# Kernel optimization log

Hardware: AMD Instinct MI355X
Metric: run time of the kernel (lower is better)

The kernel has to match this reference:

```python
import jax, jax.numpy as jnp
import numpy as np

N_BLOCKS = 4
DIN = 4000      # features per input block
DE = 128        # embed dims per block
DLAT = 512      # latent dim per block
ALPHA = 0.3     # Keras LeakyReLU default negative slope


def setup_inputs() -> dict:
    key = jax.random.key(0)
    ks = jax.random.split(key, 7)
    N = 4096
    x = jax.random.normal(ks[0], (N, N_BLOCKS * DIN), dtype=jnp.float32)
    mask = jax.random.bernoulli(ks[1], 0.5, (N, N_BLOCKS * DIN))
    embed = jax.random.normal(ks[2], (N, N_BLOCKS * DE), dtype=jnp.float32)
    batches = jax.random.normal(ks[3], (N, 8), dtype=jnp.float32)
    mean_vals = jax.random.normal(ks[4], (N_BLOCKS * DIN,), dtype=jnp.float32)
    fan_in = DIN + DE + 8
    W = jax.random.normal(ks[5], (N_BLOCKS, fan_in, DLAT), dtype=jnp.float32) / np.sqrt(fan_in)
    b = jnp.zeros((N_BLOCKS, DLAT), dtype=jnp.float32)
    return {"x": x, "mask": mask, "embed": embed, "batches": batches,
            "mean_vals": mean_vals, "W": W, "b": b}


def reference(x, mask, embed, batches, mean_vals, W, b):
    N = x.shape[0]
    db = batches.shape[1]
    # masked mean-centering: x = where(mask, x - mean, 0)
    xm = jnp.where(mask, x - mean_vals[None, :], jnp.zeros((), x.dtype))
    # equal-sized splits == reshape into [N, B, din] / [N, B, de]
    xb = xm.reshape(N, N_BLOCKS, DIN)
    eb = embed.reshape(N, N_BLOCKS, DE)
    bb = jnp.broadcast_to(batches[:, None, :], (N, N_BLOCKS, db))
    inp = jnp.concatenate([xb, eb, bb], axis=-1)  # [N, B, DIN+DE+db]
    h = jnp.einsum('nbi,bio->nbo', inp, W) + b[None, :, :]  # grouped GEMM
    h = jnp.where(h >= 0, h, ALPHA * h)  # LeakyReLU(alpha=0.3)
    return h.reshape(N, N_BLOCKS * DLAT)  # concat of per-block outputs
```

## Files before the change

### kernel.cpp

```cpp
#include <hip/hip_runtime.h>

#define NROWS 4096
#define NBLK 4
#define DIN 4000
#define DE 128
#define DB 8
#define DLAT 512
#define FANIN 4136
#define KPAD 4224
#define NKT 66
#define XC 16000
#define OUTC 2048
#define TC 192

#define PW_GRID 2112

typedef __attribute__((ext_vector_type(8))) short short8;
typedef __attribute__((ext_vector_type(4))) float floatx4;
typedef float __attribute__((ext_vector_type(4))) f32x4;
typedef int   __attribute__((ext_vector_type(4))) i32x4;

__device__ __forceinline__ unsigned short f2bf(float f) {
    unsigned int u = __builtin_bit_cast(unsigned int, f);
    u = (u + 0x7FFFu + ((u >> 16) & 1u)) >> 16;
    return (unsigned short)u;
}

__device__ __forceinline__ void async16(const void* g, void* l) {
    __builtin_amdgcn_global_load_lds(
        (const __attribute__((address_space(1))) void*)g,
        (__attribute__((address_space(3))) void*)l, 16, 0, 0);
}

__global__ void prep_w(const float* __restrict__ W, unsigned short* __restrict__ Wp) {
    __shared__ unsigned short tile[64 * 68];
    int bid = blockIdx.x;
    int nt = bid & 7;
    int t2 = bid >> 3;
    int kt = t2 % 66;
    int b  = t2 / 66;
    int tid = threadIdx.x;
    int n0 = nt * 64;
    int k0 = kt * 64;
#pragma unroll
    for (int i = 0; i < 4; ++i) {
        int c = i * 256 + tid;
        int r = c >> 4;
        int q = (c & 15) * 4;
        int pk = k0 + r;
        int wr = (pk < DIN) ? pk : ((pk >= 4032 && pk < 4168) ? pk - 32 : -1);
        float4 v = make_float4(0.f, 0.f, 0.f, 0.f);
        if (wr >= 0)
            v = *reinterpret_cast<const float4*>(W + ((size_t)b * FANIN + wr) * DLAT + n0 + q);
        ushort4 u4 = make_ushort4(f2bf(v.x), f2bf(v.y), f2bf(v.z), f2bf(v.w));
        *reinterpret_cast<ushort4*>(&tile[r * 68 + q]) = u4;
    }
    __syncthreads();
#pragma unroll
    for (int i = 0; i < 2; ++i) {
        int c = i * 256 + tid;
        int nl = c >> 3;
        int kc = c & 7;
        unsigned short o[8];
#pragma unroll
        for (int j = 0; j < 8; ++j) o[j] = tile[(kc * 8 + j) * 68 + nl];
        *reinterpret_cast<short8*>(Wp + ((size_t)(b * DLAT + n0 + nl)) * KPAD + k0 + kc * 8) =
            *reinterpret_cast<const short8*>(o);
    }
}

__global__ __launch_bounds__(512, 2) void gemm_f(
    const float* __restrict__ x, const int* __restrict__ mask,
    const float* __restrict__ mean, const float* __restrict__ embed,
    const float* __restrict__ batches, const float* __restrict__ bias,
    const unsigned short* __restrict__ Wp, float* __restrict__ out) {
    __shared__ unsigned short A0[64 * 64];
    __shared__ unsigned short A1[64 * 64];
    __shared__ unsigned short B0[512 * 64];
    __shared__ unsigned short B1[512 * 64];

    int bid = blockIdx.x;
    int b   = bid & 3;
    int mt  = bid >> 2;
    int row0 = mt * 64;
    int tid  = threadIdx.x;
    int lane = tid & 63;
    int w    = tid >> 6;
    int quad = lane >> 4;
    int l16  = lane & 15;
    int r    = tid >> 3;
    int cgl  = tid & 7;

    const unsigned short* Bbase = Wp + (size_t)b * DLAT * KPAD;

    floatx4 acc[4][4];
#pragma unroll
    for (int m = 0; m < 4; ++m)
#pragma unroll
        for (int n = 0; n < 4; ++n) acc[m][n] = (floatx4){0.f, 0.f, 0.f, 0.f};

    f32x4 xa, xb, ea, eb;
    i32x4 mka, mkb;
    int amode;

#define STAGE_B(BN, KT) do {                                                   \
    int k0_ = (KT) * 64;                                                       \
    _Pragma("unroll")                                                          \
    for (int i_ = 0; i_ < 8; ++i_) {                                           \
        int c_  = i_ * 512 + tid;                                              \
        int nl_ = c_ >> 3;                                                     \
        int cg_ = (c_ & 7) ^ (nl_ & 7);                                        \
        async16(Bbase + (size_t)nl_ * KPAD + k0_ + cg_ * 8, &BN[c_ * 8]);      \
    }                                                                          \
} while (0)

#define LOAD_A(KT) do {                                                        \
    int col_ = (KT) * 64 + cgl * 8;                                            \
    amode = 3;                                                                 \
    if (col_ < DIN) {                                                          \
        amode = 0;                                                             \
        size_t gi_ = (size_t)(row0 + r) * XC + (size_t)b * DIN + col_;         \
        const f32x4* xp_ = reinterpret_cast<const f32x4*>(x + gi_);            \
        const i32x4* mp_ = reinterpret_cast<const i32x4*>(mask + gi_);         \
        xa  = __builtin_nontemporal_load(xp_);                                 \
        xb  = __builtin_nontemporal_load(xp_ + 1);                             \
        mka = __builtin_nontemporal_load(mp_);                                 \
        mkb = __builtin_nontemporal_load(mp_ + 1);                             \
        const f32x4* ep_ = reinterpret_cast<const f32x4*>(mean + b * DIN + col_); \
        ea = ep_[0]; eb = ep_[1];                                              \
    } else if (col_ >= 4032 && col_ < 4160) {                                  \
        amode = 1;                                                             \
        const f32x4* ep_ = reinterpret_cast<const f32x4*>(                     \
            embed + (size_t)(row0 + r) * (NBLK * DE) + b * DE + (col_ - 4032)); \
        ea = ep_[0]; eb = ep_[1];                                              \
    } else if (col_ == 4160) {                                                 \
        amode = 1;                                                             \
        const f32x4* bp_ = reinterpret_cast<const f32x4*>(                     \
            batches + (size_t)(row0 + r) * DB);                                \
        ea = bp_[0]; eb = bp_[1];                                              \
    }                                                                          \
} while (0)

#define WRITE_A(AN) do {                                                       \
    short8 v8_ = (short8){0, 0, 0, 0, 0, 0, 0, 0};                             \
    if (amode == 0) {                                                          \
        float f0_ = mka.x ? xa.x - ea.x : 0.f;                                 \
        float f1_ = mka.y ? xa.y - ea.y : 0.f;                                 \
        float f2_ = mka.z ? xa.z - ea.z : 0.f;                                 \
        float f3_ = mka.w ? xa.w - ea.w : 0.f;                                 \
        float f4_ = mkb.x ? xb.x - eb.x : 0.f;                                 \
        float f5_ = mkb.y ? xb.y - eb.y : 0.f;                                 \
        float f6_ = mkb.z ? xb.z - eb.z : 0.f;                                 \
        float f7_ = mkb.w ? xb.w - eb.w : 0.f;                                 \
        v8_ = (short8){(short)f2bf(f0_), (short)f2bf(f1_), (short)f2bf(f2_),   \
                       (short)f2bf(f3_), (short)f2bf(f4_), (short)f2bf(f5_),   \
                       (short)f2bf(f6_), (short)f2bf(f7_)};                    \
    } else if (amode == 1) {                                                   \
        v8_ = (short8){(short)f2bf(ea.x), (short)f2bf(ea.y), (short)f2bf(ea.z),\
                       (short)f2bf(ea.w), (short)f2bf(eb.x), (short)f2bf(eb.y),\
                       (short)f2bf(eb.z), (short)f2bf(eb.w)};                  \
    }                                                                          \
    *reinterpret_cast<short8*>(&AN[r * 64 + ((cgl ^ (r & 7)) * 8)]) = v8_;     \
} while (0)

#define COMPUTE(AN, BN) do {                                                   \
    _Pragma("unroll")                                                          \
    for (int s_ = 0; s_ < 2; ++s_) {                                           \
        short8 af_[4], bf_[4];                                                 \
        _Pragma("unroll")                                                      \
        for (int m_ = 0; m_ < 4; ++m_) {                                       \
            int ar_ = m_ * 16 + l16;                                           \
            af_[m_] = *reinterpret_cast<const short8*>(                        \
                &AN[ar_ * 64 + (((s_ * 4 + quad) ^ (ar_ & 7)) * 8)]);          \
        }                                                                      \
        _Pragma("unroll")                                                      \
        for (int n_ = 0; n_ < 4; ++n_) {                                       \
            int br_ = w * 64 + n_ * 16 + l16;                                  \
            bf_[n_] = *reinterpret_cast<const short8*>(                        \
                &BN[br_ * 64 + (((s_ * 4 + quad) ^ (br_ & 7)) * 8)]);          \
        }                                                                      \
        _Pragma("unroll")                                                      \
        for (int m_ = 0; m_ < 4; ++m_)                                         \
            _Pragma("unroll")                                                  \
            for (int n_ = 0; n_ < 4; ++n_)                                     \
                acc[m_][n_] = __builtin_amdgcn_mfma_f32_16x16x32_bf16(         \
                    af_[m_], bf_[n_], acc[m_][n_], 0, 0, 0);                   \
    }                                                                          \
} while (0)

    LOAD_A(0);
    STAGE_B(B0, 0);
    WRITE_A(A0);
    __syncthreads();

    for (int kt = 0; kt < NKT; kt += 2) {
        LOAD_A(kt + 1);
        STAGE_B(B1, kt + 1);
        COMPUTE(A0, B0);
        WRITE_A(A1);
        __syncthreads();
        if (kt + 2 < NKT) {
            LOAD_A(kt + 2);
            STAGE_B(B0, kt + 2);
        }
        COMPUTE(A1, B1);
        if (kt + 2 < NKT) WRITE_A(A0);
        __syncthreads();
    }

#pragma unroll
    for (int m = 0; m < 4; ++m) {
#pragma unroll
        for (int n = 0; n < 4; ++n) {
            int col_l = w * 64 + n * 16 + l16;
            float bv = bias[b * DLAT + col_l];
#pragma unroll
            for (int rr = 0; rr < 4; ++rr) {
                int row_l = m * 16 + quad * 4 + rr;
                float v = acc[m][n][rr] + bv;
                v = v >= 0.f ? v : 0.3f * v;
                out[(size_t)(row0 + row_l) * OUTC + b * DLAT + col_l] = v;
            }
        }
    }
#undef STAGE_B
#undef LOAD_A
#undef WRITE_A
#undef COMPUTE
}

__global__ void prep_t(const float* __restrict__ embed, const float* __restrict__ batches,
                       unsigned short* __restrict__ T) {
    int i  = blockIdx.x * 256 + threadIdx.x;
    int t  = i % TC;
    int nb = i / TC;
    int b  = nb & 3;
    int n  = nb >> 2;
    float v = 0.f;
    if (t < DE)            v = embed[(size_t)n * (NBLK * DE) + b * DE + t];
    else if (t < DE + DB)  v = batches[(size_t)n * DB + (t - DE)];
    T[i] = f2bf(v);
}

__global__ __launch_bounds__(256, 3) void gemm_k(
    const float* __restrict__ x, const int* __restrict__ mask,
    const float* __restrict__ mean, const float* __restrict__ bias,
    const unsigned short* __restrict__ Wp, const unsigned short* __restrict__ T,
    float* __restrict__ out) {
    __shared__ unsigned short Asm_[128 * 64];
    __shared__ unsigned short Bsm_[128 * 64];

    int bid = blockIdx.x;
    int nt  = bid & 3;
    int b   = (bid >> 2) & 3;
    int mt  = bid >> 4;
    int tid  = threadIdx.x;
    int lane = tid & 63;
    int w    = tid >> 6;
    int wm   = w >> 1;
    int wn   = w & 1;
    int quad = lane >> 4;
    int l16  = lane & 15;
    int row0 = mt * 128;
    int n0   = nt * 128;

    floatx4 acc[4][4];
#pragma unroll
    for (int m = 0; m < 4; ++m)
#pragma unroll
        for (int n = 0; n < 4; ++n) acc[m][n] = (floatx4){0.f, 0.f, 0.f, 0.f};

    for (int kt = 0; kt < NKT; ++kt) {
        if (kt < 63) {
#pragma unroll
            for (int i = 0; i < 4; ++i) {
                int c  = i * 256 + tid;
                int r  = c >> 3;
                int cg = c & 7;
                int col = kt * 64 + cg * 8;
                short8 v8 = (short8){0, 0, 0, 0, 0, 0, 0, 0};
                if (col < DIN) {
                    size_t gi = (size_t)(row0 + r) * XC + (size_t)b * DIN + col;
                    const float4* xp = reinterpret_cast<const float4*>(x + gi);
                    const int4*   mp = reinterpret_cast<const int4*>(mask + gi);
                    const float4* ep = reinterpret_cast<const float4*>(mean + b * DIN + col);
                    float4 x0 = xp[0], x1 = xp[1];
                    int4   m0 = mp[0], m1 = mp[1];
                    float4 e0 = ep[0], e1 = ep[1];
                    float f0 = m0.x ? x0.x - e0.x : 0.f;
                    float f1 = m0.y ? x0.y - e0.y : 0.f;
                    float f2 = m0.z ? x0.z - e0.z : 0.f;
                    float f3 = m0.w ? x0.w - e0.w : 0.f;
                    float f4 = m1.x ? x1.x - e1.x : 0.f;
                    float f5 = m1.y ? x1.y - e1.y : 0.f;
                    float f6 = m1.z ? x1.z - e1.z : 0.f;
                    float f7 = m1.w ? x1.w - e1.w : 0.f;
                    v8 = (short8){(short)f2bf(f0), (short)f2bf(f1), (short)f2bf(f2),
                                  (short)f2bf(f3), (short)f2bf(f4), (short)f2bf(f5),
                                  (short)f2bf(f6), (short)f2bf(f7)};
                }
                *reinterpret_cast<short8*>(&Asm_[r * 64 + ((cg ^ (r & 7)) * 8)]) = v8;
            }
        } else {
#pragma unroll
            for (int i = 0; i < 4; ++i) {
                int c  = i * 256 + tid;
                int r  = c >> 3;
                int cg = (c & 7) ^ (r & 7);
                async16(T + ((size_t)(row0 + r) * NBLK + b) * TC + (kt - 63) * 64 + cg * 8,
                        &Asm_[c * 8]);
            }
        }
#pragma unroll
        for (int i = 0; i < 4; ++i) {
            int c  = i * 256 + tid;
            int nl = c >> 3;
            int cg = (c & 7) ^ (nl & 7);
            async16(Wp + ((size_t)(b * DLAT + n0 + nl)) * KPAD + kt * 64 + cg * 8,
                    &Bsm_[c * 8]);
        }
        __syncthreads();
#pragma unroll
        for (int s = 0; s < 2; ++s) {
            short8 af[4], bfr[4];
#pragma unroll
            for (int m = 0; m < 4; ++m) {
                int ar = wm * 64 + m * 16 + l16;
                af[m] = *reinterpret_cast<const short8*>(
                    &Asm_[ar * 64 + (((s * 4 + quad) ^ (ar & 7)) * 8)]);
            }
#pragma unroll
            for (int n = 0; n < 4; ++n) {
                int br = wn * 64 + n * 16 + l16;
                bfr[n] = *reinterpret_cast<const short8*>(
                    &Bsm_[br * 64 + (((s * 4 + quad) ^ (br & 7)) * 8)]);
            }
#pragma unroll
            for (int m = 0; m < 4; ++m)
#pragma unroll
                for (int n = 0; n < 4; ++n)
                    acc[m][n] = __builtin_amdgcn_mfma_f32_16x16x32_bf16(
                        af[m], bfr[n], acc[m][n], 0, 0, 0);
        }
        __syncthreads();
    }

#pragma unroll
    for (int m = 0; m < 4; ++m) {
#pragma unroll
        for (int n = 0; n < 4; ++n) {
            int col_l = wn * 64 + n * 16 + l16;
            float bv = bias[b * DLAT + n0 + col_l];
#pragma unroll
            for (int r = 0; r < 4; ++r) {
                int row_l = wm * 64 + m * 16 + quad * 4 + r;
                float v = acc[m][n][r] + bv;
                v = v >= 0.f ? v : 0.3f * v;
                out[(size_t)(row0 + row_l) * OUTC + b * DLAT + n0 + col_l] = v;
            }
        }
    }
}

extern "C" void kernel_launch(void* const* d_in, const int* in_sizes, int n_in,
                              void* d_out, int out_size, void* d_ws, size_t ws_size,
                              hipStream_t stream) {
    const float* x       = (const float*)d_in[0];
    const int*   mask    = (const int*)d_in[1];
    const float* embed   = (const float*)d_in[2];
    const float* batches = (const float*)d_in[3];
    const float* mean    = (const float*)d_in[4];
    const float* W       = (const float*)d_in[5];
    const float* bias    = (const float*)d_in[6];
    float* out = (float*)d_out;

    unsigned short* Wp = (unsigned short*)d_ws;
    size_t wp_elems = (size_t)NBLK * DLAT * KPAD;
    size_t wp_bytes = wp_elems * 2;

    prep_w<<<dim3(PW_GRID), dim3(256), 0, stream>>>(W, Wp);

    if (ws_size >= wp_bytes + (size_t)(NROWS * NBLK * TC) * 2) {
        gemm_f<<<dim3(256), dim3(512), 0, stream>>>(
            x, mask, mean, embed, batches, bias, Wp, out);
    } else {
        unsigned short* T = Wp + wp_elems;
        prep_t<<<dim3(12288), dim3(256), 0, stream>>>(embed, batches, T);
        gemm_k<<<dim3(512), dim3(256), 0, stream>>>(x, mask, mean, bias, Wp, T, out);
    }
}
```

Measured before the change: 601.3 us.

## Precompute tail A tiles in prep kernel and hand-schedule GEMM pipeline waits

The weight-prep kernel now also writes a bf16 tensor holding the last four K-tiles of A: the final masked-x columns, embed and batches. The GEMM reads those tiles with async LDS loads, so its main loop no longer carries the branchy amode logic. The main loop is restructured to issue the next A global load before the barrier. It replaces __syncthreads with explicit vmcnt/lgkmcnt waits and sched_barriers, which lets loads stay in flight across the MFMA phase. This adds some extra workspace traffic, and the manual waitcnt counts have to match the exact number of outstanding loads.

Result: faster. 584.7 us (-2.8%).

```diff
diff --git a/kernel.cpp b/kernel.cpp
--- a/kernel.cpp
+++ b/kernel.cpp
@@ -12,8 +12,10 @@
 #define XC 16000
 #define OUTC 2048
 #define TC 192
+#define T2C 256
 
 #define PW_GRID 2112
+#define PT2_GRID 2048
 
 typedef __attribute__((ext_vector_type(8))) short short8;
 typedef __attribute__((ext_vector_type(4))) float floatx4;
@@ -32,48 +34,101 @@
         (__attribute__((address_space(3))) void*)l, 16, 0, 0);
 }
 
-__global__ void prep_w(const float* __restrict__ W, unsigned short* __restrict__ Wp) {
+#define SCHED0 __builtin_amdgcn_sched_barrier(0)
+#define BAR    __builtin_amdgcn_s_barrier()
+#define WAITVM6 asm volatile("s_waitcnt vmcnt(6)" ::: "memory")
+#define WAITVM0 asm volatile("s_waitcnt vmcnt(0)" ::: "memory")
+#define WAITLG  asm volatile("s_waitcnt lgkmcnt(0)" ::: "memory")
+
+__global__ void prep_wt(const float* __restrict__ W, unsigned short* __restrict__ Wp,
+                        const float* __restrict__ x, const int* __restrict__ mask,
+                        const float* __restrict__ mean, const float* __restrict__ embed,
+                        const float* __restrict__ batches, unsigned short* __restrict__ T2) {
     __shared__ unsigned short tile[64 * 68];
     int bid = blockIdx.x;
-    int nt = bid & 7;
-    int t2 = bid >> 3;
-    int kt = t2 % 66;
-    int b  = t2 / 66;
     int tid = threadIdx.x;
-    int n0 = nt * 64;
-    int k0 = kt * 64;
-#pragma unroll
-    for (int i = 0; i < 4; ++i) {
-        int c = i * 256 + tid;
-        int r = c >> 4;
-        int q = (c & 15) * 4;
-        int pk = k0 + r;
-        int wr = (pk < DIN) ? pk : ((pk >= 4032 && pk < 4168) ? pk - 32 : -1);
-        float4 v = make_float4(0.f, 0.f, 0.f, 0.f);
-        if (wr >= 0)
-            v = *reinterpret_cast<const float4*>(W + ((size_t)b * FANIN + wr) * DLAT + n0 + q);
-        ushort4 u4 = make_ushort4(f2bf(v.x), f2bf(v.y), f2bf(v.z), f2bf(v.w));
-        *reinterpret_cast<ushort4*>(&tile[r * 68 + q]) = u4;
-    }
-    __syncthreads();
-#pragma unroll
-    for (int i = 0; i < 2; ++i) {
-        int c = i * 256 + tid;
-        int nl = c >> 3;
-        int kc = c & 7;
-        unsigned short o[8];
-#pragma unroll
-        for (int j = 0; j < 8; ++j) o[j] = tile[(kc * 8 + j) * 68 + nl];
-        *reinterpret_cast<short8*>(Wp + ((size_t)(b * DLAT + n0 + nl)) * KPAD + k0 + kc * 8) =
-            *reinterpret_cast<const short8*>(o);
-    }
+
+    if (bid < PW_GRID) {
+        int nt = bid & 7;
+        int t2 = bid >> 3;
+        int kt = t2 % 66;
+        int b  = t2 / 66;
+        int n0 = nt * 64;
+        int k0 = kt * 64;
+#pragma unroll
+        for (int i = 0; i < 4; ++i) {
+            int c = i * 256 + tid;
+            int r = c >> 4;
+            int q = (c & 15) * 4;
+            int pk = k0 + r;
+            int wr = (pk < DIN) ? pk : ((pk >= 4032 && pk < 4168) ? pk - 32 : -1);
+            float4 v = make_float4(0.f, 0.f, 0.f, 0.f);
+            if (wr >= 0)
+                v = *reinterpret_cast<const float4*>(W + ((size_t)b * FANIN + wr) * DLAT + n0 + q);
+            ushort4 u4 = make_ushort4(f2bf(v.x), f2bf(v.y), f2bf(v.z), f2bf(v.w));
+            *reinterpret_cast<ushort4*>(&tile[r * 68 + q]) = u4;
+        }
+        __syncthreads();
+#pragma unroll
+        for (int i = 0; i < 2; ++i) {
+            int c = i * 256 + tid;
+            int nl = c >> 3;
+            int kc = c & 7;
+            unsigned short o[8];
+#pragma unroll
+            for (int j = 0; j < 8; ++j) o[j] = tile[(kc * 8 + j) * 68 + nl];
+            *reinterpret_cast<short8*>(Wp + ((size_t)(b * DLAT + n0 + nl)) * KPAD + k0 + kc * 8) =
+                *reinterpret_cast<const short8*>(o);
+        }
+        return;
+    }
+
+    int i  = (bid - PW_GRID) * 256 + tid;
+    int tc = i & 31;
+    int rb = i >> 5;
+    int b  = rb & 3;
+    int row = rb >> 2;
+    int k  = tc * 8;
+    short8 v8 = (short8){0, 0, 0, 0, 0, 0, 0, 0};
+    if (k < 32) {
+        int col = 3968 + k;
+        size_t gi = (size_t)row * XC + (size_t)b * DIN + col;
+        const f32x4* xp = reinterpret_cast<const f32x4*>(x + gi);
+        const i32x4* mp = reinterpret_cast<const i32x4*>(mask + gi);
+        const f32x4* ep = reinterpret_cast<const f32x4*>(mean + b * DIN + col);
+        f32x4 x0 = xp[0], x1 = xp[1];
+        i32x4 m0 = mp[0], m1 = mp[1];
+        f32x4 e0 = ep[0], e1 = ep[1];
+        float f0 = m0.x ? x0.x - e0.x : 0.f;
+        float f1 = m0.y ? x0.y - e0.y : 0.f;
+        float f2 = m0.z ? x0.z - e0.z : 0.f;
+        float f3 = m0.w ? x0.w - e0.w : 0.f;
+        float f4 = m1.x ? x1.x - e1.x : 0.f;
+        float f5 = m1.y ? x1.y - e1.y : 0.f;
+        float f6 = m1.z ? x1.z - e1.z : 0.f;
+        float f7 = m1.w ? x1.w - e1.w : 0.f;
+        v8 = (short8){(short)f2bf(f0), (short)f2bf(f1), (short)f2bf(f2), (short)f2bf(f3),
+                      (short)f2bf(f4), (short)f2bf(f5), (short)f2bf(f6), (short)f2bf(f7)};
+    } else if (k >= 64 && k < 192) {
+        const f32x4* ep = reinterpret_cast<const f32x4*>(
+            embed + (size_t)row * (NBLK * DE) + b * DE + (k - 64));
+        f32x4 a = ep[0], bb = ep[1];
+        v8 = (short8){(short)f2bf(a.x), (short)f2bf(a.y), (short)f2bf(a.z), (short)f2bf(a.w),
+                      (short)f2bf(bb.x), (short)f2bf(bb.y), (short)f2bf(bb.z), (short)f2bf(bb.w)};
+    } else if (k == 192) {
+        const f32x4* bp = reinterpret_cast<const f32x4*>(batches + (size_t)row * DB);
+        f32x4 a = bp[0], bb = bp[1];
+        v8 = (short8){(short)f2bf(a.x), (short)f2bf(a.y), (short)f2bf(a.z), (short)f2bf(a.w),
+                      (short)f2bf(bb.x), (short)f2bf(bb.y), (short)f2bf(bb.z), (short)f2bf(bb.w)};
+    }
+    *reinterpret_cast<short8*>(T2 + (size_t)rb * T2C + k) = v8;
 }
 
 __global__ __launch_bounds__(512, 2) void gemm_f(
     const float* __restrict__ x, const int* __restrict__ mask,
-    const float* __restrict__ mean, const float* __restrict__ embed,
-    const float* __restrict__ batches, const float* __restrict__ bias,
-    const unsigned short* __restrict__ Wp, float* __restrict__ out) {
+    const float* __restrict__ mean, const float* __restrict__ bias,
+    const unsigned short* __restrict__ Wp, const unsigned short* __restrict__ T2,
+    float* __restrict__ out) {
     __shared__ unsigned short A0[64 * 64];
     __shared__ unsigned short A1[64 * 64];
     __shared__ unsigned short B0[512 * 64];
@@ -101,7 +156,6 @@
 
     f32x4 xa, xb, ea, eb;
     i32x4 mka, mkb;
-    int amode;
 
 #define STAGE_B(BN, KT) do {                                                   \
     int k0_ = (KT) * 64;                                                       \
@@ -114,52 +168,37 @@
     }                                                                          \
 } while (0)
 
+#define STAGE_T(AN, KT) do {                                                   \
+    async16(T2 + ((size_t)(row0 + r) * NBLK + b) * T2C + ((KT) - 62) * 64 +    \
+                ((cgl ^ (r & 7)) * 8),                                         \
+            &AN[tid * 8]);                                                     \
+} while (0)
+
 #define LOAD_A(KT) do {                                                        \
     int col_ = (KT) * 64 + cgl * 8;                                            \
-    amode = 3;                                                                 \
-    if (col_ < DIN) {                                                          \
-        amode = 0;                                                             \
-        size_t gi_ = (size_t)(row0 + r) * XC + (size_t)b * DIN + col_;         \
-        const f32x4* xp_ = reinterpret_cast<const f32x4*>(x + gi_);            \
-        const i32x4* mp_ = reinterpret_cast<const i32x4*>(mask + gi_);         \
-        xa  = __builtin_nontemporal_load(xp_);                                 \
-        xb  = __builtin_nontemporal_load(xp_ + 1);                             \
-        mka = __builtin_nontemporal_load(mp_);                                 \
-        mkb = __builtin_nontemporal_load(mp_ + 1);                             \
-        const f32x4* ep_ = reinterpret_cast<const f32x4*>(mean + b * DIN + col_); \
-        ea = ep_[0]; eb = ep_[1];                                              \
-    } else if (col_ >= 4032 && col_ < 4160) {                                  \
-        amode = 1;                                                             \
-        const f32x4* ep_ = reinterpret_cast<const f32x4*>(                     \
-            embed + (size_t)(row0 + r) * (NBLK * DE) + b * DE + (col_ - 4032)); \
-        ea = ep_[0]; eb = ep_[1];                                              \
-    } else if (col_ == 4160) {                                                 \
-        amode = 1;                                                             \
-        const f32x4* bp_ = reinterpret_cast<const f32x4*>(                     \
-            batches + (size_t)(row0 + r) * DB);                                \
-        ea = bp_[0]; eb = bp_[1];                                              \
-    }                                                                          \
+    size_t gi_ = (size_t)(row0 + r) * XC + (size_t)b * DIN + col_;             \
+    const f32x4* xp_ = reinterpret_cast<const f32x4*>(x + gi_);                \
+    const i32x4* mp_ = reinterpret_cast<const i32x4*>(mask + gi_);             \
+    xa  = __builtin_nontemporal_load(xp_);                                     \
+    xb  = __builtin_nontemporal_load(xp_ + 1);                                 \
+    mka = __builtin_nontemporal_load(mp_);                                     \
+    mkb = __builtin_nontemporal_load(mp_ + 1);                                 \
+    const f32x4* ep_ = reinterpret_cast<const f32x4*>(mean + b * DIN + col_);  \
+    ea = ep_[0]; eb = ep_[1];                                                  \
 } while (0)
 
 #define WRITE_A(AN) do {                                                       \
-    short8 v8_ = (short8){0, 0, 0, 0, 0, 0, 0, 0};                             \
-    if (amode == 0) {                                                          \
-        float f0_ = mka.x ? xa.x - ea.x : 0.f;                                 \
-        float f1_ = mka.y ? xa.y - ea.y : 0.f;                                 \
-        float f2_ = mka.z ? xa.z - ea.z : 0.f;                                 \
-        float f3_ = mka.w ? xa.w - ea.w : 0.f;                                 \
-        float f4_ = mkb.x ? xb.x - eb.x : 0.f;                                 \
-        float f5_ = mkb.y ? xb.y - eb.y : 0.f;                                 \
-        float f6_ = mkb.z ? xb.z - eb.z : 0.f;                                 \
-        float f7_ = mkb.w ? xb.w - eb.w : 0.f;                                 \
-        v8_ = (short8){(short)f2bf(f0_), (short)f2bf(f1_), (short)f2bf(f2_),   \
-                       (short)f2bf(f3_), (short)f2bf(f4_), (short)f2bf(f5_),   \
-                       (short)f2bf(f6_), (short)f2bf(f7_)};                    \
-    } else if (amode == 1) {                                                   \
-        v8_ = (short8){(short)f2bf(ea.x), (short)f2bf(ea.y), (short)f2bf(ea.z),\
-                       (short)f2bf(ea.w), (short)f2bf(eb.x), (short)f2bf(eb.y),\
-                       (short)f2bf(eb.z), (short)f2bf(eb.w)};                  \
-    }                                                                          \
+    float f0_ = mka.x ? xa.x - ea.x : 0.f;                                     \
+    float f1_ = mka.y ? xa.y - ea.y : 0.f;                                     \
+    float f2_ = mka.z ? xa.z - ea.z : 0.f;                                     \
+    float f3_ = mka.w ? xa.w - ea.w : 0.f;                                     \
+    float f4_ = mkb.x ? xb.x - eb.x : 0.f;                                     \
+    float f5_ = mkb.y ? xb.y - eb.y : 0.f;                                     \
+    float f6_ = mkb.z ? xb.z - eb.z : 0.f;                                     \
+    float f7_ = mkb.w ? xb.w - eb.w : 0.f;                                     \
+    short8 v8_ = (short8){(short)f2bf(f0_), (short)f2bf(f1_), (short)f2bf(f2_),\
+                          (short)f2bf(f3_), (short)f2bf(f4_), (short)f2bf(f5_),\
+                          (short)f2bf(f6_), (short)f2bf(f7_)};                 \
     *reinterpret_cast<short8*>(&AN[r * 64 + ((cgl ^ (r & 7)) * 8)]) = v8_;     \
 } while (0)
 
@@ -190,23 +229,64 @@
 
     LOAD_A(0);
     STAGE_B(B0, 0);
+    SCHED0;
     WRITE_A(A0);
-    __syncthreads();
-
-    for (int kt = 0; kt < NKT; kt += 2) {
-        LOAD_A(kt + 1);
+    SCHED0;
+    LOAD_A(1);
+    SCHED0;
+    WAITVM6;
+    WAITLG;
+    BAR;
+    SCHED0;
+
+    for (int kt = 0; kt < 60; kt += 2) {
         STAGE_B(B1, kt + 1);
+        SCHED0;
         COMPUTE(A0, B0);
         WRITE_A(A1);
-        __syncthreads();
-        if (kt + 2 < NKT) {
-            LOAD_A(kt + 2);
-            STAGE_B(B0, kt + 2);
-        }
+        SCHED0;
+        LOAD_A(kt + 2);
+        SCHED0;
+        WAITVM6;
+        WAITLG;
+        BAR;
+        SCHED0;
+        STAGE_B(B0, kt + 2);
+        SCHED0;
         COMPUTE(A1, B1);
-        if (kt + 2 < NKT) WRITE_A(A0);
-        __syncthreads();
-    }
+        WRITE_A(A0);
+        SCHED0;
+        LOAD_A(kt + 3);
+        SCHED0;
+        WAITVM6;
+        WAITLG;
+        BAR;
+        SCHED0;
+    }
+
+    STAGE_B(B1, 61);
+    SCHED0;
+    COMPUTE(A0, B0);
+    WRITE_A(A1);
+    SCHED0;
+    WAITVM0;
+    WAITLG;
+    BAR;
+    SCHED0;
+
+    STAGE_T(A0, 62); STAGE_B(B0, 62); SCHED0;
+    COMPUTE(A1, B1);
+    WAITVM0; WAITLG; BAR; SCHED0;
+    STAGE_T(A1, 63); STAGE_B(B1, 63); SCHED0;
+    COMPUTE(A0, B0);
+    WAITVM0; WAITLG; BAR; SCHED0;
+    STAGE_T(A0, 64); STAGE_B(B0, 64); SCHED0;
+    COMPUTE(A1, B1);
+    WAITVM0; WAITLG; BAR; SCHED0;
+    STAGE_T(A1, 65); STAGE_B(B1, 65); SCHED0;
+    COMPUTE(A0, B0);
+    WAITVM0; WAITLG; BAR; SCHED0;
+    COMPUTE(A1, B1);
 
 #pragma unroll
     for (int m = 0; m < 4; ++m) {
@@ -224,9 +304,47 @@
         }
     }
 #undef STAGE_B
+#undef STAGE_T
 #undef LOAD_A
 #undef WRITE_A
 #undef COMPUTE
+}
+
+__global__ void prep_w(const float* __restrict__ W, unsigned short* __restrict__ Wp) {
+    __shared__ unsigned short tile[64 * 68];
+    int bid = blockIdx.x;
+    int nt = bid & 7;
+    int t2 = bid >> 3;
+    int kt = t2 % 66;
+    int b  = t2 / 66;
+    int tid = threadIdx.x;
+    int n0 = nt * 64;
+    int k0 = kt * 64;
+#pragma unroll
+    for (int i = 0; i < 4; ++i) {
+        int c = i * 256 + tid;
+        int r = c >> 4;
+        int q = (c & 15) * 4;
+        int pk = k0 + r;
+        int wr = (pk < DIN) ? pk : ((pk >= 4032 && pk < 4168) ? pk - 32 : -1);
+        float4 v = make_float4(0.f, 0.f, 0.f, 0.f);
+        if (wr >= 0)
+            v = *reinterpret_cast<const float4*>(W + ((size_t)b * FANIN + wr) * DLAT + n0 + q);
+        ushort4 u4 = make_ushort4(f2bf(v.x), f2bf(v.y), f2bf(v.z), f2bf(v.w));
+        *reinterpret_cast<ushort4*>(&tile[r * 68 + q]) = u4;
+    }
+    __syncthreads();
+#pragma unroll
+    for (int i = 0; i < 2; ++i) {
+        int c = i * 256 + tid;
+        int nl = c >> 3;
+        int kc = c & 7;
+        unsigned short o[8];
+#pragma unroll
+        for (int j = 0; j < 8; ++j) o[j] = tile[(kc * 8 + j) * 68 + nl];
+        *reinterpret_cast<short8*>(Wp + ((size_t)(b * DLAT + n0 + nl)) * KPAD + k0 + kc * 8) =
+            *reinterpret_cast<const short8*>(o);
+    }
 }
 
 __global__ void prep_t(const float* __restrict__ embed, const float* __restrict__ batches,
@@ -376,14 +494,17 @@
 
     unsigned short* Wp = (unsigned short*)d_ws;
     size_t wp_elems = (size_t)NBLK * DLAT * KPAD;
-    size_t wp_bytes = wp_elems * 2;
-
-    prep_w<<<dim3(PW_GRID), dim3(256), 0, stream>>>(W, Wp);
-
-    if (ws_size >= wp_bytes + (size_t)(NROWS * NBLK * TC) * 2) {
+    size_t t2_elems = (size_t)NROWS * NBLK * T2C;
+    size_t need_fast = (wp_elems + t2_elems) * 2;
+
+    if (ws_size >= need_fast) {
+        unsigned short* T2 = Wp + wp_elems;
+        prep_wt<<<dim3(PW_GRID + PT2_GRID), dim3(256), 0, stream>>>(
+            W, Wp, x, mask, mean, embed, batches, T2);
         gemm_f<<<dim3(256), dim3(512), 0, stream>>>(
-            x, mask, mean, embed, batches, bias, Wp, out);
+            x, mask, mean, bias, Wp, T2, out);
     } else {
+        prep_w<<<dim3(PW_GRID), dim3(256), 0, stream>>>(W, Wp);
         unsigned short* T = Wp + wp_elems;
         prep_t<<<dim3(12288), dim3(256), 0, stream>>>(embed, batches, T);
         gemm_k<<<dim3(512), dim3(256), 0, stream>>>(x, mask, mean, bias, Wp, T, out);
```
